# Kernel tuning notes

Measured on AMD Instinct MI355X. Metric: run time of the kernel, lower is better.

## Reference

```python
import jax, jax.numpy as jnp
import numpy as np
from jax import lax

DN = ('NCHW', 'OIHW', 'NCHW')

def _conv(x, w, b, stride, pad):
    y = lax.conv_general_dilated(x, w, (stride, stride), [(pad, pad), (pad, pad)], dimension_numbers=DN)
    return y + b[None, :, None, None]

def _resblock(x, w1, b1, w2, b2, wd, bd, stride):
    # standard pre-activation-free ResNet block: conv3x3(stride)-ReLU-conv3x3 + 1x1(stride) skip, final ReLU
    identity = _conv(x, wd, bd, stride, 0)
    h = jax.nn.relu(_conv(x, w1, b1, stride, 1))
    h = _conv(h, w2, b2, 1, 1)
    return jax.nn.relu(h + identity)

def _deconv(x, w, b, stride, out_pad):
    # PyTorch ConvTranspose2d(k=3, padding=1, output_padding=out_pad) as dilated conv
    # w has PyTorch layout (in_ch, out_ch, kH, kW) -> flip spatially, swap to OIHW
    wt = jnp.flip(w, (2, 3)).transpose(1, 0, 2, 3)
    y = lax.conv_general_dilated(x, wt, (1, 1), [(1, 1 + out_pad), (1, 1 + out_pad)], lhs_dilation=(stride, stride), dimension_numbers=DN)
    return y + b[None, :, None, None]

def _quantize(enc, codebook):
    # enc: (B, C, H, W); codebook: (N, C). Squared-Euclidean distances, argmin, lookup.
    e = enc.transpose(0, 2, 3, 1)  # (B, H, W, C)
    d = (jnp.sum(e * e, axis=-1, keepdims=True)
         - 2.0 * jnp.einsum('bhwc,nc->bhwn', e, codebook)
         + jnp.sum(codebook * codebook, axis=-1))  # (B, H, W, N)
    idx = jnp.argmin(d, axis=-1)
    q = codebook[idx]  # (B, H, W, C)
    return q.transpose(0, 3, 1, 2)

def setup_inputs() -> dict:
    key = jax.random.key(0)
    ks = jax.random.split(key, 28)
    def W(k, shape):
        return jax.random.normal(k, shape, jnp.float32) * 0.05
    inp = {"x": jax.random.normal(ks[0], (32, 3, 256, 256), jnp.float32)}
    enc_chans = [(3, 64), (64, 128), (128, 64)]
    i = 1
    for l, (cin, cout) in enumerate(enc_chans):
        inp[f"enc{l}_w1"] = W(ks[i], (cout, cin, 3, 3))
        inp[f"enc{l}_b1"] = W(ks[i + 1], (cout,))
        inp[f"enc{l}_w2"] = W(ks[i + 2], (cout, cout, 3, 3))
        inp[f"enc{l}_b2"] = W(ks[i + 3], (cout,))
        inp[f"enc{l}_wd"] = W(ks[i + 4], (cout, cin, 1, 1))
        inp[f"enc{l}_bd"] = W(ks[i + 5], (cout,))
        i += 6
    # decoder ConvTranspose2d weights in PyTorch layout (in_ch, out_ch, 3, 3)
    dec_chans = [(64, 128), (128, 64), (64, 3)]
    for l, (cin, cout) in enumerate(dec_chans):
        inp[f"dec{l}_w"] = W(ks[i], (cin, cout, 3, 3))
        inp[f"dec{l}_b"] = W(ks[i + 1], (cout,))
        i += 2
    inp["codebook"] = W(ks[i], (512, 64))
    return inp

def reference(x, enc0_w1, enc0_b1, enc0_w2, enc0_b2, enc0_wd, enc0_bd,
              enc1_w1, enc1_b1, enc1_w2, enc1_b2, enc1_wd, enc1_bd,
              enc2_w1, enc2_b1, enc2_w2, enc2_b2, enc2_wd, enc2_bd,
              dec0_w, dec0_b, dec1_w, dec1_b, dec2_w, dec2_b, codebook):
    # encode: 256 -> 128 -> 64 -> 64 spatially
    h = _resblock(x, enc0_w1, enc0_b1, enc0_w2, enc0_b2, enc0_wd, enc0_bd, 2)
    h = _resblock(h, enc1_w1, enc1_b1, enc1_w2, enc1_b2, enc1_wd, enc1_bd, 2)
    h = _resblock(h, enc2_w1, enc2_b1, enc2_w2, enc2_b2, enc2_wd, enc2_bd, 1)
    q = _quantize(h, codebook)
    # decode with output_size matching encoder input shapes (output_padding: 0, 1, 1)
    h = jax.nn.relu(_deconv(q, dec0_w, dec0_b, 1, 0))   # 64 -> 64
    h = jax.nn.relu(_deconv(h, dec1_w, dec1_b, 2, 1))   # 64 -> 128
    return _deconv(h, dec2_w, dec2_b, 2, 1)             # 128 -> 256
```

## Files before the change

kernel.cpp:

```cpp
#include <hip/hip_runtime.h>
#include <cstddef>


typedef float v4f __attribute__((ext_vector_type(4)));
typedef _Float16 f16x8 __attribute__((ext_vector_type(8)));
typedef _Float16 f16x4 __attribute__((ext_vector_type(4)));

__device__ __forceinline__ void fma4(v4f& a, float p, const v4f& w) {
    a.x = fmaf(p, w.x, a.x); a.y = fmaf(p, w.y, a.y);
    a.z = fmaf(p, w.z, a.z); a.w = fmaf(p, w.w, a.w);
}

__global__ void repack_k(const float* __restrict__ src, float* __restrict__ dst,
                         int cout, int coutR, int cin, int flip, int deconv)
{
    int t = blockIdx.x * 256 + threadIdx.x;
    int tot = cin * 9 * cout;
    if (t >= tot) return;
    int co = t % cout; int k = (t / cout) % 9; int ci = t / (9 * cout);
    float v = 0.f;
    if (co < coutR) {
        int ks = flip ? 8 - k : k;
        v = deconv ? src[((size_t)ci * coutR + co) * 9 + ks]
                   : src[((size_t)co * cin + ci) * 9 + ks];
    }
    dst[t] = v;
}

__global__ void repackB16_k(const float* __restrict__ src, _Float16* __restrict__ bh,
                            _Float16* __restrict__ bl, int COUT, int CIN, int deconv)
{
    int t = blockIdx.x * 256 + threadIdx.x;
    int tot = 9 * CIN * COUT;
    if (t >= tot) return;
    int NGtot = COUT >> 4, C32 = CIN >> 5;
    int j = t & 7;
    int lane = (t >> 3) & 63;
    int blk = t >> 9;
    int ng = blk % NGtot; blk /= NGtot;
    int c32 = blk % C32;
    int tap = blk / C32;
    int co = ng * 16 + (lane & 15);
    int ci = c32 * 32 + ((lane >> 4) & 3) * 8 + j;
    float v = deconv ? src[((size_t)ci * COUT + co) * 9 + (8 - tap)]
                     : src[((size_t)co * CIN + ci) * 9 + tap];
    _Float16 h = (_Float16)v;
    _Float16 l = (_Float16)(v - (float)h);
    bh[t] = h; bl[t] = l;
}

__global__ void repackQ_k(const float* __restrict__ cb, _Float16* __restrict__ qb)
{
    int t = blockIdx.x * 256 + threadIdx.x;
    if (t >= 65536) return;
    int j = t & 7;
    int lane = (t >> 3) & 63;
    int hl = (t >> 9) & 1;
    int s = (t >> 10) & 1;
    int nt = t >> 11;
    int code = nt * 16 + (lane & 15);
    int ci = s * 32 + ((lane >> 4) & 3) * 8 + j;
    float v = cb[(size_t)code * 64 + ci];
    _Float16 h = (_Float16)v;
    qb[t] = hl ? (_Float16)(v - (float)h) : h;
}

__global__ void cbnorm_k(const float* __restrict__ cb, float* __restrict__ cn)
{
    int i = blockIdx.x * 256 + threadIdx.x;
    if (i >= 512) return;
    float s = 0.f;
#pragma unroll
    for (int j = 0; j < 64; ++j) { float v = cb[i * 64 + j]; s = fmaf(v, v, s); }
    cn[i] = s;
}

template<int CIN, bool RELU, int ADDMODE, bool CLIN, bool CLOUT>
__launch_bounds__(256, 2)
__global__ void mconv3s1_k(const float* __restrict__ in,
                           const _Float16* __restrict__ Bh, const _Float16* __restrict__ Bl,
                           const float* __restrict__ bias, float* __restrict__ out,
                           const float* __restrict__ addend,
                           int COUT, int H, int W)
{
    constexpr int C32 = CIN / 32;
    __shared__ __align__(16) unsigned char smBuf[76416];
    _Float16* AH = (_Float16*)smBuf;
    _Float16* AL = AH + 12960;
    _Float16* BW = AL + 12960;
    float* smO = (float*)smBuf;

    const int tid = threadIdx.x;
    const int lane = tid & 63, yb = tid >> 6;
    const int n16 = lane & 15, q = lane >> 4;

    int b = blockIdx.x;
    const int chunks = COUT >> 6;
    const int coch = b % chunks; b /= chunks;
    const int tX = W >> 4; const int tx = b % tX; b /= tX;
    const int tY = H >> 4; const int ty = b % tY; const int n = b / tY;
    const int x0 = tx * 16, y0 = ty * 16;
    const int NGtot = COUT >> 4;
    const int ngbase = coch * 4, cobase = coch * 64;

    v4f acc[4][4];
#pragma unroll
    for (int ng = 0; ng < 4; ++ng) {
        float bb = bias[cobase + ng * 16 + n16];
        v4f bv = {bb, bb, bb, bb};
#pragma unroll
        for (int mg = 0; mg < 4; ++mg) acc[mg][ng] = bv;
    }

    for (int c32 = 0; c32 < C32; ++c32) {
        __syncthreads();
        if (CLIN) {
            for (int u = tid; u < 2592; u += 256) {
                int cell = u >> 3, f4 = u & 7;
                int yy = cell / 18, xx = cell - yy * 18;
                int gy = y0 - 1 + yy, gx = x0 - 1 + xx;
                float4 v = make_float4(0.f, 0.f, 0.f, 0.f);
                if (gy >= 0 && gy < H && gx >= 0 && gx < W)
                    v = *(const float4*)&in[(((size_t)n * H + gy) * W + gx) * CIN + c32 * 32 + f4 * 4];
                f16x4 h4, l4;
                h4[0] = (_Float16)v.x; l4[0] = (_Float16)(v.x - (float)h4[0]);
                h4[1] = (_Float16)v.y; l4[1] = (_Float16)(v.y - (float)h4[1]);
                h4[2] = (_Float16)v.z; l4[2] = (_Float16)(v.z - (float)h4[2]);
                h4[3] = (_Float16)v.w; l4[3] = (_Float16)(v.w - (float)h4[3]);
                int a = (yy * 18 + xx) * 40 + f4 * 4;
                *(f16x4*)&AH[a] = h4; *(f16x4*)&AL[a] = l4;
            }
        } else {
            for (int u = tid; u < 10368; u += 256) {
                int ci = u / 324, rem = u - ci * 324;
                int yy = rem / 18, xx = rem - yy * 18;
                int gy = y0 - 1 + yy, gx = x0 - 1 + xx;
                float v = 0.f;
                if (gy >= 0 && gy < H && gx >= 0 && gx < W)
                    v = in[(((size_t)n * CIN + c32 * 32 + ci) * H + gy) * W + gx];
                _Float16 h = (_Float16)v;
                _Float16 l = (_Float16)(v - (float)h);
                int a = (yy * 18 + xx) * 40 + ci;
                AH[a] = h; AL[a] = l;
            }
        }
        for (int ky = 0; ky < 3; ++ky) {
            __syncthreads();
            for (int u = tid; u < 1536; u += 256) {
                int lu = u & 63;
                int rest = u >> 6;
                int hl = rest & 1; rest >>= 1;
                int ng = rest & 3;
                int tapL = rest >> 2;
                const uint4* srcp = (const uint4*)(hl ? Bl : Bh);
                size_t sidx = (((size_t)(ky * 3 + tapL) * C32 + c32) * NGtot + ngbase + ng) * 64 + lu;
                ((uint4*)BW)[u] = srcp[sidx];
            }
            __syncthreads();
#pragma unroll
            for (int kx = 0; kx < 3; ++kx) {
                f16x8 aH[4], aL[4];
#pragma unroll
                for (int mg = 0; mg < 4; ++mg) {
                    int aoff = ((4 * yb + mg + ky) * 18 + n16 + kx) * 40 + q * 8;
                    aH[mg] = *(const f16x8*)&AH[aoff];
                    aL[mg] = *(const f16x8*)&AL[aoff];
                }
#pragma unroll
                for (int ng = 0; ng < 4; ++ng) {
                    int boff = ((kx * 4 + ng) * 2) * 512 + lane * 8;
                    f16x8 bH = *(const f16x8*)&BW[boff];
                    f16x8 bL = *(const f16x8*)&BW[boff + 512];
#pragma unroll
                    for (int mg = 0; mg < 4; ++mg) {
                        acc[mg][ng] = __builtin_amdgcn_mfma_f32_16x16x32_f16(aH[mg], bH, acc[mg][ng], 0, 0, 0);
                        acc[mg][ng] = __builtin_amdgcn_mfma_f32_16x16x32_f16(aL[mg], bH, acc[mg][ng], 0, 0, 0);
                        acc[mg][ng] = __builtin_amdgcn_mfma_f32_16x16x32_f16(aH[mg], bL, acc[mg][ng], 0, 0, 0);
                    }
                }
            }
        }
    }

    __syncthreads();
#pragma unroll
    for (int mg = 0; mg < 4; ++mg)
#pragma unroll
        for (int ng = 0; ng < 4; ++ng) {
            int p = (4 * yb + mg) * 16 + q * 4;
            int co = ng * 16 + n16;
#pragma unroll
            for (int r = 0; r < 4; ++r)
                smO[co * 257 + p + r] = acc[mg][ng][r];
        }
    __syncthreads();
    if (CLOUT) {
        const int p = tid;
        const int py = p >> 4, px = p & 15;
        size_t cellBase = (((size_t)n * H + (y0 + py)) * W + (x0 + px)) * COUT + cobase;
        float* cellp = out + cellBase;
        const float* acell = (ADDMODE == 2) ? addend + cellBase : nullptr;
#pragma unroll
        for (int g = 0; g < 16; ++g) {
            float4 v;
            v.x = smO[(4 * g + 0) * 257 + p];
            v.y = smO[(4 * g + 1) * 257 + p];
            v.z = smO[(4 * g + 2) * 257 + p];
            v.w = smO[(4 * g + 3) * 257 + p];
            if (ADDMODE == 2) {
                float4 a4 = *(const float4*)&acell[4 * g];
                v.x += a4.x; v.y += a4.y; v.z += a4.z; v.w += a4.w;
            }
            if (RELU) {
                v.x = fmaxf(v.x, 0.f); v.y = fmaxf(v.y, 0.f);
                v.z = fmaxf(v.z, 0.f); v.w = fmaxf(v.w, 0.f);
            }
            *(float4*)&cellp[4 * g] = v;
        }
    } else {
        const size_t plane = (size_t)H * W;
        float* ob = out + ((size_t)n * COUT + cobase) * plane;
        const float* ab = (ADDMODE == 1) ? addend + ((size_t)n * COUT + cobase) * plane : nullptr;
#pragma unroll
        for (int k = 0; k < 64; ++k) {
            int e = tid + 256 * k;
            int co = e >> 8, p = e & 255;
            int py = p >> 4, px = p & 15;
            size_t g = (size_t)co * plane + (size_t)(y0 + py) * W + x0 + px;
            float v = smO[co * 257 + p];
            if (ADDMODE == 1) v += ab[g];
            if (RELU) v = fmaxf(v, 0.f);
            ob[g] = v;
        }
    }
}

template<int CIN, int NG, bool RELU>
__launch_bounds__(256, 2)
__global__ void mconv3s2_k(const float* __restrict__ in,
                           const _Float16* __restrict__ Bh, const _Float16* __restrict__ Bl,
                           const float* __restrict__ bias, float* __restrict__ out,
                           int COUT, int Hin, int Win)
{
    constexpr int C32 = CIN / 32;
    constexpr int ASZ = 9 * 2 * 17 * 40;
    __shared__ __align__(16) unsigned char smBuf[(2 * ASZ + NG * 1024) * 2];
    _Float16* AH = (_Float16*)smBuf;
    _Float16* AL = AH + ASZ;
    _Float16* BW = AL + ASZ;
    float* smO = (float*)smBuf;

    const int tid = threadIdx.x;
    const int lane = tid & 63, yb = tid >> 6;
    const int n16 = lane & 15, q = lane >> 4;

    const int Hout = Hin >> 1, Wout = Win >> 1;
    int b = blockIdx.x;
    const int chunks = COUT / (NG * 16);
    const int coch = b % chunks; b /= chunks;
    const int tX = Wout >> 4; const int tx = b % tX; b /= tX;
    const int tY = Hout >> 2; const int ty = b % tY; const int n = b / tY;
    const int x0 = tx * 16, y0 = ty * 4;
    const int gx0 = 2 * x0 - 1, gy0 = 2 * y0 - 1;
    const int NGtot = COUT >> 4;
    const int ngbase = coch * NG, cobase = coch * NG * 16;

    v4f acc[NG];
#pragma unroll
    for (int ng = 0; ng < NG; ++ng) {
        float bb = bias[cobase + ng * 16 + n16];
        v4f bv = {bb, bb, bb, bb};
        acc[ng] = bv;
    }

    for (int c32 = 0; c32 < C32; ++c32) {
        __syncthreads();
        for (int u = tid; u < 9504; u += 256) {
            int ci = u / 297, rem = u - ci * 297;
            int yy = rem / 33, xx = rem - yy * 33;
            int gy = gy0 + yy, gx = gx0 + xx;
            float v = 0.f;
            if (gy >= 0 && gy < Hin && gx >= 0 && gx < Win)
                v = in[(((size_t)n * CIN + c32 * 32 + ci) * Hin + gy) * Win + gx];
            _Float16 h = (_Float16)v;
            _Float16 l = (_Float16)(v - (float)h);
            int a = ((yy * 2 + (xx & 1)) * 17 + (xx >> 1)) * 40 + ci;
            AH[a] = h; AL[a] = l;
        }
#pragma unroll
        for (int ky = 0; ky < 3; ++ky) {
#pragma unroll
            for (int kx = 0; kx < 3; ++kx) {
                __syncthreads();
                for (int u = tid; u < NG * 128; u += 256) {
                    int lu = u & 63;
                    int rest = u >> 6;
                    int hl = rest & 1;
                    int ng = rest >> 1;
                    const uint4* srcp = (const uint4*)(hl ? Bl : Bh);
                    size_t sidx = (((size_t)(ky * 3 + kx) * C32 + c32) * NGtot + ngbase + ng) * 64 + lu;
                    ((uint4*)BW)[u] = srcp[sidx];
                }
                __syncthreads();
                const int par = kx & 1, xs = kx >> 1;
                int aoff = (((2 * yb + ky) * 2 + par) * 17 + n16 + xs) * 40 + q * 8;
                f16x8 aH = *(const f16x8*)&AH[aoff];
                f16x8 aL = *(const f16x8*)&AL[aoff];
#pragma unroll
                for (int ng = 0; ng < NG; ++ng) {
                    int boff = ng * 1024 + lane * 8;
                    f16x8 bH = *(const f16x8*)&BW[boff];
                    f16x8 bL = *(const f16x8*)&BW[boff + 512];
                    acc[ng] = __builtin_amdgcn_mfma_f32_16x16x32_f16(aH, bH, acc[ng], 0, 0, 0);
                    acc[ng] = __builtin_amdgcn_mfma_f32_16x16x32_f16(aL, bH, acc[ng], 0, 0, 0);
                    acc[ng] = __builtin_amdgcn_mfma_f32_16x16x32_f16(aH, bL, acc[ng], 0, 0, 0);
                }
            }
        }
    }

    __syncthreads();
#pragma unroll
    for (int ng = 0; ng < NG; ++ng) {
        int co = ng * 16 + n16;
        int p = yb * 16 + q * 4;
#pragma unroll
        for (int r = 0; r < 4; ++r)
            smO[co * 65 + p + r] = acc[ng][r];
    }
    __syncthreads();
    const int p2 = tid >> 2, s2 = tid & 3;
    const int py = p2 >> 4, px = p2 & 15;
    float* cellp = out + ((((size_t)n * Hout + (y0 + py)) * Wout + (x0 + px)) * COUT + s2 * 32);
#pragma unroll
    for (int k = 0; k < 8; ++k) {
        float4 v;
        v.x = smO[(s2 * 32 + 4 * k + 0) * 65 + p2];
        v.y = smO[(s2 * 32 + 4 * k + 1) * 65 + p2];
        v.z = smO[(s2 * 32 + 4 * k + 2) * 65 + p2];
        v.w = smO[(s2 * 32 + 4 * k + 3) * 65 + p2];
        if (RELU) {
            v.x = fmaxf(v.x, 0.f); v.y = fmaxf(v.y, 0.f);
            v.z = fmaxf(v.z, 0.f); v.w = fmaxf(v.w, 0.f);
        }
        *(float4*)&cellp[4 * k] = v;
    }
}

template<int CIN, bool RELU>
__launch_bounds__(256, 3)
__global__ void mdeconv2_k(const float* __restrict__ in,
                           const _Float16* __restrict__ Bh, const _Float16* __restrict__ Bl,
                           const float* __restrict__ bias, float* __restrict__ out,
                           int COUT, int Hin, int Win)
{
    constexpr int C32 = CIN / 32;
    __shared__ __align__(16) unsigned char smBuf[38976];
    _Float16* AH = (_Float16*)smBuf;
    _Float16* AL = AH + 3600;
    _Float16* BW = AL + 3600;
    float* smO = (float*)smBuf;

    const int tid = threadIdx.x;
    const int lane = tid & 63, yb = tid >> 6;
    const int n16 = lane & 15, q = lane >> 4;

    int b = blockIdx.x;
    const int chunks = COUT >> 6;
    const int coch = b % chunks; b /= chunks;
    const int tX = Win >> 4; const int tx = b % tX; b /= tX;
    const int tY = Hin >> 2; const int ty = b % tY; const int n = b / tY;
    const int x0 = tx * 16, y0 = ty * 4;
    const int NGtot = COUT >> 4;
    const int ngbase = coch * 4, cobase = coch * 64;

    v4f acc[4][4];
#pragma unroll
    for (int ng = 0; ng < 4; ++ng) {
        float bb = bias[cobase + ng * 16 + n16];
        v4f bv = {bb, bb, bb, bb};
#pragma unroll
        for (int ph = 0; ph < 4; ++ph) acc[ph][ng] = bv;
    }

    for (int c32 = 0; c32 < C32; ++c32) {
        __syncthreads();
        for (int u = tid; u < 680; u += 256) {
            int cell = u >> 3, f4 = u & 7;
            int yy = cell / 17, xx = cell - yy * 17;
            int gy = y0 + yy, gx = x0 + xx;
            float4 v = make_float4(0.f, 0.f, 0.f, 0.f);
            if (gy < Hin && gx < Win)
                v = *(const float4*)&in[(((size_t)n * Hin + gy) * Win + gx) * CIN + c32 * 32 + f4 * 4];
            f16x4 h4, l4;
            h4[0] = (_Float16)v.x; l4[0] = (_Float16)(v.x - (float)h4[0]);
            h4[1] = (_Float16)v.y; l4[1] = (_Float16)(v.y - (float)h4[1]);
            h4[2] = (_Float16)v.z; l4[2] = (_Float16)(v.z - (float)h4[2]);
            h4[3] = (_Float16)v.w; l4[3] = (_Float16)(v.w - (float)h4[3]);
            int a = (yy * 18 + xx) * 40 + f4 * 4;
            *(f16x4*)&AH[a] = h4; *(f16x4*)&AL[a] = l4;
        }
        for (int ky = 0; ky < 3; ++ky) {
            __syncthreads();
            for (int u = tid; u < 1536; u += 256) {
                int lu = u & 63;
                int rest = u >> 6;
                int hl = rest & 1; rest >>= 1;
                int ng = rest & 3;
                int tapL = rest >> 2;
                const uint4* srcp = (const uint4*)(hl ? Bl : Bh);
                size_t sidx = (((size_t)(ky * 3 + tapL) * C32 + c32) * NGtot + ngbase + ng) * 64 + lu;
                ((uint4*)BW)[u] = srcp[sidx];
            }
            __syncthreads();
            const int iy = (ky == 2) ? 1 : 0;
            const int phy = (ky == 1) ? 0 : 2;
#pragma unroll
            for (int kx = 0; kx < 3; ++kx) {
                const int ix = (kx == 2) ? 1 : 0;
                const int ph = phy + ((kx == 1) ? 0 : 1);
                int aoff = ((yb + iy) * 18 + n16 + ix) * 40 + q * 8;
                f16x8 aH = *(const f16x8*)&AH[aoff];
                f16x8 aL = *(const f16x8*)&AL[aoff];
#pragma unroll
                for (int ng = 0; ng < 4; ++ng) {
                    int boff = ((kx * 4 + ng) * 2) * 512 + lane * 8;
                    f16x8 bH = *(const f16x8*)&BW[boff];
                    f16x8 bL = *(const f16x8*)&BW[boff + 512];
                    acc[ph][ng] = __builtin_amdgcn_mfma_f32_16x16x32_f16(aH, bH, acc[ph][ng], 0, 0, 0);
                    acc[ph][ng] = __builtin_amdgcn_mfma_f32_16x16x32_f16(aL, bH, acc[ph][ng], 0, 0, 0);
                    acc[ph][ng] = __builtin_amdgcn_mfma_f32_16x16x32_f16(aH, bL, acc[ph][ng], 0, 0, 0);
                }
            }
        }
    }

    const int Wout = Win * 2;
    const size_t plane = (size_t)(Hin * 2) * (size_t)Wout;
    float* ob = out + ((size_t)n * COUT + cobase) * plane;
    const int oy0 = 2 * y0, ox0 = 2 * x0;
#pragma unroll
    for (int half = 0; half < 2; ++half) {
        __syncthreads();
#pragma unroll
        for (int ph = 0; ph < 4; ++ph) {
            const int dy = ph >> 1, dx = ph & 1;
#pragma unroll
            for (int g = 0; g < 2; ++g) {
                int ng = half * 2 + g;
#pragma unroll
                for (int r = 0; r < 4; ++r)
                    smO[(g * 16 + n16) * 257 + (2 * yb + dy) * 32 + 2 * (q * 4 + r) + dx] = acc[ph][ng][r];
            }
        }
        __syncthreads();
#pragma unroll
        for (int k = 0; k < 32; ++k) {
            int pos = tid;
            int oyl = pos >> 5, oxl = pos & 31;
            float v = smO[k * 257 + pos];
            if (RELU) v = fmaxf(v, 0.f);
            ob[(size_t)(half * 32 + k) * plane + (size_t)(oy0 + oyl) * Wout + ox0 + oxl] = v;
        }
    }
}

template<int CIN, int CB, bool RELU>
__launch_bounds__(256, 4)
__global__ void conv3s2_k(const float* __restrict__ in, const float* __restrict__ wp,
                          const float* __restrict__ bias, float* __restrict__ out,
                          int COUT, int Hin, int Win)
{
    constexpr int COC = 32;
    __shared__ float smIn[CB * 2178];
    __shared__ float smW[CB * 9 * COC];
    const int Hout = Hin >> 1, Wout = Win >> 1;
    const int tid = threadIdx.x;
    int b = blockIdx.x;
    const int chunks = COUT / COC;
    const int tX = Wout / 32, tY = Hout / 16;
    const int ch = b % chunks; b /= chunks;
    const int tx = b % tX; b /= tX;
    const int ty = b % tY; const int n = b / tY;
    const int cobase = ch * COC;
    const int r = tid >> 4, c = tid & 15;
    const int gy0 = ty * 32 - 1, gx0 = tx * 64 - 1;

    v4f acc[16];
#pragma unroll
    for (int g = 0; g < 8; ++g) {
        v4f bv = *(const v4f*)&bias[cobase + 4 * g];
        acc[g] = bv; acc[8 + g] = bv;
    }

    const size_t plane = (size_t)Hin * Win;
    const float* ip0 = in + (size_t)n * CIN * plane;
    const float* wp0 = wp + cobase;

    for (int ci0 = 0; ci0 < CIN; ci0 += CB) {
        __syncthreads();
        for (int idx = tid; idx < CB * 2178; idx += 256) {
            int ci = idx / 2178, rem = idx - ci * 2178;
            int rr = rem / 66, cc = rem - rr * 66;
            int gy = gy0 + rr, gx = gx0 + cc;
            float v = 0.f;
            if (gy >= 0 && gy < Hin && gx >= 0 && gx < Win)
                v = ip0[(size_t)(ci0 + ci) * plane + (size_t)gy * Win + gx];
            smIn[idx] = v;
        }
        for (int idx = tid; idx < CB * 9 * COC; idx += 256) {
            int q2 = idx >> 5, co = idx & 31;
            smW[idx] = wp0[((size_t)ci0 * 9 + q2) * COUT + co];
        }
        __syncthreads();

#pragma unroll 1
        for (int ci = 0; ci < CB; ++ci) {
            float p[15];
            const float* sp = &smIn[ci * 2178 + 2 * r * 66 + 4 * c];
#pragma unroll
            for (int i = 0; i < 3; ++i)
#pragma unroll
                for (int j = 0; j < 5; ++j)
                    p[i * 5 + j] = sp[i * 66 + j];
            const float* wrow = &smW[ci * 288];
#pragma unroll
            for (int k = 0; k < 9; ++k) {
                const int ky = k / 3, kx = k % 3;
#pragma unroll
                for (int g = 0; g < 8; ++g) {
                    v4f wv = *(const v4f*)&wrow[k * 32 + 4 * g];
                    fma4(acc[g],     p[ky * 5 + kx],     wv);
                    fma4(acc[8 + g], p[ky * 5 + kx + 2], wv);
                }
            }
        }
    }

    const int oy = ty * 16 + r, ox = tx * 32 + 2 * c;
    size_t cellBase = (((size_t)n * Hout + oy) * Wout + ox) * COUT + cobase;
#pragma unroll
    for (int g = 0; g < 8; ++g) {
        v4f v0 = acc[g], v1 = acc[8 + g];
        if (RELU) {
#pragma unroll
            for (int e = 0; e < 4; ++e) { v0[e] = fmaxf(v0[e], 0.f); v1[e] = fmaxf(v1[e], 0.f); }
        }
        *(v4f*)&out[cellBase + 4 * g] = v0;
        *(v4f*)&out[cellBase + COUT + 4 * g] = v1;
    }
}

template<int CIN, int CB, int COC, bool RELU>
__launch_bounds__(256, 3)
__global__ void deconv2_k(const float* __restrict__ in, const float* __restrict__ wp,
                          const float* __restrict__ bias, float* __restrict__ out,
                          int COUTR, int COUTP, int Hin, int Win)
{
    constexpr int RW = 33, RH = 17;
    __shared__ float smIn[CB * RH * RW];
    __shared__ float smW[CB * 9 * COC];
    const int Wout = Win * 2;
    const int tid = threadIdx.x;
    int b = blockIdx.x;
    const int chunks = COUTP / COC;
    const int qTX = Win / 32, qTY = Hin / 16;
    const int ch = b % chunks; b /= chunks;
    const int qtx = b % qTX; b /= qTX;
    const int qty = b % qTY; const int n = b / qTY;
    const int cobase = ch * COC;
    const int tqy = tid >> 4, tqx = tid & 15;
    const int qby = qty * 16, qbx = qtx * 32;

    v4f acc[8 * COC / 4];
#pragma unroll
    for (int g = 0; g < COC / 4; ++g) {
        v4f bv;
#pragma unroll
        for (int e = 0; e < 4; ++e)
            bv[e] = (cobase + 4 * g + e < COUTR) ? bias[cobase + 4 * g + e] : 0.f;
#pragma unroll
        for (int pt = 0; pt < 8; ++pt) acc[pt * (COC / 4) + g] = bv;
    }

    const size_t plane = (size_t)Hin * Win;
    const float* ip0 = in + (size_t)n * CIN * plane;
    const float* wp0 = wp + cobase;

    for (int ci0 = 0; ci0 < CIN; ci0 += CB) {
        __syncthreads();
        for (int idx = tid; idx < CB * RH * RW; idx += 256) {
            int ci = idx / (RH * RW), rem = idx - ci * (RH * RW);
            int rr = rem / RW, cc = rem - rr * RW;
            int gy = qby + rr, gx = qbx + cc;
            float v = 0.f;
            if (gy < Hin && gx < Win)
                v = ip0[(size_t)(ci0 + ci) * plane + (size_t)gy * Win + gx];
            smIn[idx] = v;
        }
        for (int idx = tid; idx < CB * 9 * COC; idx += 256) {
            int q2 = idx / COC, co = idx % COC;
            smW[idx] = wp0[((size_t)ci0 * 9 + q2) * COUTP + co];
        }
        __syncthreads();

#pragma unroll 1
        for (int ci = 0; ci < CB; ++ci) {
            float p[6];
            const float* sp = &smIn[ci * RH * RW + tqy * RW + 2 * tqx];
#pragma unroll
            for (int i = 0; i < 2; ++i)
#pragma unroll
                for (int j = 0; j < 3; ++j)
                    p[i * 3 + j] = sp[i * RW + j];
            const float* wrow = &smW[ci * 9 * COC];
#pragma unroll
            for (int k = 0; k < 9; ++k) {
                const int ky = k / 3, kx = k % 3;
                const int dy = (ky == 1) ? 0 : 1, iy = (ky == 0) ? 1 : 0;
                const int dx = (kx == 1) ? 0 : 1, ix = (kx == 0) ? 1 : 0;
#pragma unroll
                for (int g = 0; g < COC / 4; ++g) {
                    v4f wv = *(const v4f*)&wrow[k * COC + 4 * g];
                    fma4(acc[(0 + dy * 2 + dx) * (COC / 4) + g], p[iy * 3 + ix],     wv);
                    fma4(acc[(4 + dy * 2 + dx) * (COC / 4) + g], p[iy * 3 + ix + 1], wv);
                }
            }
        }
    }

    const size_t oPlane = (size_t)(Hin * 2) * Wout;
    const int oy = 2 * (qby + tqy), ox = 2 * (qbx + 2 * tqx);
#pragma unroll
    for (int g = 0; g < COC / 4; ++g)
#pragma unroll
        for (int e = 0; e < 4; ++e) {
            int cch = cobase + 4 * g + e;
            if (cch >= COUTR) break;
            float* op = out + ((size_t)n * COUTR + cch) * oPlane + (size_t)oy * Wout + ox;
#pragma unroll
            for (int a2 = 0; a2 < 2; ++a2) {
                float u0 = acc[(0 + a2 * 2 + 0) * (COC / 4) + g][e];
                float u1 = acc[(0 + a2 * 2 + 1) * (COC / 4) + g][e];
                float u2 = acc[(4 + a2 * 2 + 0) * (COC / 4) + g][e];
                float u3 = acc[(4 + a2 * 2 + 1) * (COC / 4) + g][e];
                if (RELU) { u0 = fmaxf(u0, 0.f); u1 = fmaxf(u1, 0.f);
                            u2 = fmaxf(u2, 0.f); u3 = fmaxf(u3, 0.f); }
                *(float4*)&op[(size_t)a2 * Wout] = make_float4(u0, u1, u2, u3);
            }
        }
}

template<int CIN, int S, bool RELU, bool CLOUT>
__launch_bounds__(256, 4)
__global__ void conv1x1_k(const float* __restrict__ in, const float* __restrict__ w,
                          const float* __restrict__ bias, float* __restrict__ out,
                          int COUT, int Hin, int Win, int Hout, int Wout)
{
    constexpr int COC = 32;
    __shared__ float smW[CIN * COC];
    const int tid = threadIdx.x;
    int b = blockIdx.x;
    const int chunks = COUT / COC;
    const int spB = (Hout * Wout) / 256;
    const int ch = b % chunks; b /= chunks;
    const int sb = b % spB; const int n = b / spB;
    const int cobase = ch * COC;

    for (int idx = tid; idx < CIN * COC; idx += 256) {
        int ci = idx / COC, co = idx - ci * COC;
        smW[idx] = w[(size_t)(cobase + co) * CIN + ci];
    }
    __syncthreads();

    const int pos = sb * 256 + tid;
    const int oy = pos / Wout, ox = pos - oy * Wout;

    v4f acc[8];
#pragma unroll
    for (int g = 0; g < 8; ++g) acc[g] = *(const v4f*)&bias[cobase + 4 * g];

    const size_t inPlane = (size_t)Hin * Win;
    const float* ip = in + (size_t)n * CIN * inPlane + (size_t)(oy * S) * Win + (size_t)(ox * S);
#pragma unroll 1
    for (int ci = 0; ci < CIN; ++ci) {
        float v = ip[(size_t)ci * inPlane];
#pragma unroll
        for (int g = 0; g < 8; ++g)
            fma4(acc[g], v, *(const v4f*)&smW[ci * COC + 4 * g]);
    }
    const size_t outPlane = (size_t)Hout * Wout;
    if (CLOUT) {
        size_t cb2 = ((size_t)n * outPlane + pos) * COUT + cobase;
#pragma unroll
        for (int g = 0; g < 8; ++g) {
            v4f v = acc[g];
            if (RELU) {
#pragma unroll
                for (int e = 0; e < 4; ++e) v[e] = fmaxf(v[e], 0.f);
            }
            *(v4f*)&out[cb2 + 4 * g] = v;
        }
    } else {
        float* op = out + ((size_t)n * COUT + cobase) * outPlane + pos;
#pragma unroll
        for (int g = 0; g < 8; ++g)
#pragma unroll
            for (int e = 0; e < 4; ++e) {
                float v = acc[g][e];
                if (RELU) v = fmaxf(v, 0.f);
                op[(size_t)(4 * g + e) * outPlane] = v;
            }
    }
}

__launch_bounds__(256, 4)
__global__ void mquant_k(const float* __restrict__ h, const _Float16* __restrict__ QB,
                         const float* __restrict__ cn, const float* __restrict__ cb,
                         float* __restrict__ q)
{
    __shared__ __align__(16) _Float16 AF[2][8192];
    __shared__ float cns[512];
    __shared__ int bidxs[128];

    const int tid = threadIdx.x;
    const int lane = tid & 63;
    const int wv = tid >> 6;
    const int n16 = lane & 15, qq = lane >> 4;

    const int n = blockIdx.x >> 5;
    const int rem0 = (blockIdx.x & 31) << 7;

    for (int u = tid; u < 1024; u += 256) {
        int posL = u >> 3, grp = u & 7;
        const float* gp = h + ((size_t)n * 4096 + rem0 + posL) * 64 + grp * 8;
        float4 v0 = *(const float4*)gp;
        float4 v1 = *(const float4*)(gp + 4);
        f16x8 hh, ll;
        hh[0] = (_Float16)v0.x; ll[0] = (_Float16)(v0.x - (float)hh[0]);
        hh[1] = (_Float16)v0.y; ll[1] = (_Float16)(v0.y - (float)hh[1]);
        hh[2] = (_Float16)v0.z; ll[2] = (_Float16)(v0.z - (float)hh[2]);
        hh[3] = (_Float16)v0.w; ll[3] = (_Float16)(v0.w - (float)hh[3]);
        hh[4] = (_Float16)v1.x; ll[4] = (_Float16)(v1.x - (float)hh[4]);
        hh[5] = (_Float16)v1.y; ll[5] = (_Float16)(v1.y - (float)hh[5]);
        hh[6] = (_Float16)v1.z; ll[6] = (_Float16)(v1.z - (float)hh[6]);
        hh[7] = (_Float16)v1.w; ll[7] = (_Float16)(v1.w - (float)hh[7]);
        int mt = posL >> 4, s = grp >> 2, qv = grp & 3;
        int a = ((mt * 2 + s) * 64 + (posL & 15) + qv * 16) * 8;
        *(f16x8*)&AF[0][a] = hh;
        *(f16x8*)&AF[1][a] = ll;
    }
    for (int u = tid; u < 512; u += 256) cns[u] = cn[u];
    __syncthreads();

    f16x8 aH[2][2], aL[2][2];
#pragma unroll
    for (int m = 0; m < 2; ++m)
#pragma unroll
        for (int s = 0; s < 2; ++s) {
            int a = (((wv * 2 + m) * 2 + s) * 64 + lane) * 8;
            aH[m][s] = *(const f16x8*)&AF[0][a];
            aL[m][s] = *(const f16x8*)&AF[1][a];
        }

    float best[2][4]; int bi[2][4];
#pragma unroll
    for (int m = 0; m < 2; ++m)
#pragma unroll
        for (int r = 0; r < 4; ++r) { best[m][r] = 3.4e38f; bi[m][r] = 0; }

    const uint4* qbp = (const uint4*)QB;
#pragma unroll 1
    for (int nt = 0; nt < 32; ++nt) {
        uint4 rH0 = qbp[((nt * 2 + 0) * 2 + 0) * 64 + lane];
        uint4 rL0 = qbp[((nt * 2 + 0) * 2 + 1) * 64 + lane];
        uint4 rH1 = qbp[((nt * 2 + 1) * 2 + 0) * 64 + lane];
        uint4 rL1 = qbp[((nt * 2 + 1) * 2 + 1) * 64 + lane];
        f16x8 bH0 = *(const f16x8*)&rH0;
        f16x8 bL0 = *(const f16x8*)&rL0;
        f16x8 bH1 = *(const f16x8*)&rH1;
        f16x8 bL1 = *(const f16x8*)&rL1;
        float cnv = cns[nt * 16 + n16];
        const int code = nt * 16 + n16;
#pragma unroll
        for (int m = 0; m < 2; ++m) {
            v4f acc = {0.f, 0.f, 0.f, 0.f};
            acc = __builtin_amdgcn_mfma_f32_16x16x32_f16(aH[m][0], bH0, acc, 0, 0, 0);
            acc = __builtin_amdgcn_mfma_f32_16x16x32_f16(aL[m][0], bH0, acc, 0, 0, 0);
            acc = __builtin_amdgcn_mfma_f32_16x16x32_f16(aH[m][0], bL0, acc, 0, 0, 0);
            acc = __builtin_amdgcn_mfma_f32_16x16x32_f16(aH[m][1], bH1, acc, 0, 0, 0);
            acc = __builtin_amdgcn_mfma_f32_16x16x32_f16(aL[m][1], bH1, acc, 0, 0, 0);
            acc = __builtin_amdgcn_mfma_f32_16x16x32_f16(aH[m][1], bL1, acc, 0, 0, 0);
#pragma unroll
            for (int r = 0; r < 4; ++r) {
                float d = fmaf(-2.f, acc[r], cnv);
                if (d < best[m][r]) { best[m][r] = d; bi[m][r] = code; }
            }
        }
    }

#pragma unroll
    for (int m = 0; m < 2; ++m)
#pragma unroll
        for (int r = 0; r < 4; ++r) {
#pragma unroll
            for (int msk = 1; msk < 16; msk <<= 1) {
                float ob = __shfl_xor(best[m][r], msk);
                int oi = __shfl_xor(bi[m][r], msk);
                if (ob < best[m][r] || (ob == best[m][r] && oi < bi[m][r])) {
                    best[m][r] = ob; bi[m][r] = oi;
                }
            }
            if (n16 == 0) bidxs[wv * 32 + m * 16 + qq * 4 + r] = bi[m][r];
        }
    __syncthreads();

    const int p = tid & 127, jh = tid >> 7;
    const int code = bidxs[p];
    const float4* crow4 = (const float4*)(cb + (size_t)code * 64);
    float4* qp4 = (float4*)(q + ((size_t)n * 4096 + rem0 + p) * 64);
#pragma unroll
    for (int k = 0; k < 8; ++k)
        qp4[jh * 8 + k] = crow4[jh * 8 + k];
}

extern "C" void kernel_launch(void* const* d_in, const int* in_sizes, int n_in,
                              void* d_out, int out_size, void* d_ws, size_t ws_size,
                              hipStream_t stream)
{
    const float* x    = (const float*)d_in[0];
    const float* e0w1 = (const float*)d_in[1];  const float* e0b1 = (const float*)d_in[2];
    const float* e0w2 = (const float*)d_in[3];  const float* e0b2 = (const float*)d_in[4];
    const float* e0wd = (const float*)d_in[5];  const float* e0bd = (const float*)d_in[6];
    const float* e1w1 = (const float*)d_in[7];  const float* e1b1 = (const float*)d_in[8];
    const float* e1w2 = (const float*)d_in[9];  const float* e1b2 = (const float*)d_in[10];
    const float* e1wd = (const float*)d_in[11]; const float* e1bd = (const float*)d_in[12];
    const float* e2w1 = (const float*)d_in[13]; const float* e2b1 = (const float*)d_in[14];
    const float* e2w2 = (const float*)d_in[15]; const float* e2b2 = (const float*)d_in[16];
    const float* e2wd = (const float*)d_in[17]; const float* e2bd = (const float*)d_in[18];
    const float* d0w  = (const float*)d_in[19]; const float* d0b  = (const float*)d_in[20];
    const float* d1w  = (const float*)d_in[21]; const float* d1b  = (const float*)d_in[22];
    const float* d2w  = (const float*)d_in[23]; const float* d2b  = (const float*)d_in[24];
    const float* cb   = (const float*)d_in[25];
    float* out = (float*)d_out;
    float* ws  = (float*)d_ws;

    float* P_e0w1 = out + 0;
    _Float16* Bh_d1   = (_Float16*)(out + 1728);
    _Float16* Bl_d1   = (_Float16*)(out + 38592);
    _Float16* Bh_e0c2 = (_Float16*)(out + 77760);
    _Float16* Bl_e0c2 = (_Float16*)(out + 96192);
    _Float16* Bh_e1c2 = (_Float16*)(out + 114624);
    _Float16* Bl_e1c2 = (_Float16*)(out + 188352);
    _Float16* Bh_e2c1 = (_Float16*)(out + 262080);
    _Float16* Bl_e2c1 = (_Float16*)(out + 298944);
    _Float16* Bh_e2c2 = (_Float16*)(out + 335808);
    _Float16* Bl_e2c2 = (_Float16*)(out + 354240);
    _Float16* Bh_d0   = (_Float16*)(out + 372672);
    _Float16* Bl_d0   = (_Float16*)(out + 409536);
    _Float16* Bh_e1c1 = (_Float16*)(out + 446400);
    _Float16* Bl_e1c1 = (_Float16*)(out + 483264);
    _Float16* QB = (_Float16*)(out + 520128);
    float* CN = out + 552896;
    float* P_d2w  = ws + 50405376;

    float* S0 = ws;
    float* T1 = ws + 33554432;
    float* T3 = ws + 33554432;
    float* S1 = ws + 50331648;
    float* S2 = ws;
    float* T5 = ws + 8388608;
    float* Q  = ws + 16777216;
    float* D0 = ws + 33554432;
    float* D1 = ws;

    dim3 blk(256);
    auto rp = [&](const float* src, float* dst, int cout, int coutR, int cin, int flip, int dec) {
        int tot = cin * 9 * cout;
        repack_k<<<dim3((tot + 255) / 256), blk, 0, stream>>>(src, dst, cout, coutR, cin, flip, dec);
    };
    auto rpB = [&](const float* src, _Float16* bh, _Float16* bl, int cout, int cin, int dec) {
        int tot = 9 * cin * cout;
        repackB16_k<<<dim3((tot + 255) / 256), blk, 0, stream>>>(src, bh, bl, cout, cin, dec);
    };

    rp(e0w1, P_e0w1, 64, 64, 3, 0, 0);
    rpB(e0w2, Bh_e0c2, Bl_e0c2, 64, 64, 0);
    rpB(e1w1, Bh_e1c1, Bl_e1c1, 128, 64, 0);
    rpB(e1w2, Bh_e1c2, Bl_e1c2, 128, 128, 0);
    rpB(e2w1, Bh_e2c1, Bl_e2c1, 64, 128, 0);
    rpB(e2w2, Bh_e2c2, Bl_e2c2, 64, 64, 0);
    rpB(d0w,  Bh_d0,   Bl_d0,   128, 64, 1);
    rpB(d1w,  Bh_d1,   Bl_d1,   64, 128, 1);
    repackQ_k<<<dim3(256), blk, 0, stream>>>(cb, QB);
    cbnorm_k<<<dim3(2), blk, 0, stream>>>(cb, CN);

    conv1x1_k<3, 2, false, false><<<dim3(32 * 64 * 2), blk, 0, stream>>>(
        x, e0wd, e0bd, S0, 64, 256, 256, 128, 128);
    conv3s2_k<3, 3, true><<<dim3(32 * 8 * 4 * 2), blk, 0, stream>>>(
        x, P_e0w1, e0b1, T1, 64, 256, 256);
    mconv3s1_k<64, true, 1, true, false><<<dim3(32 * 8 * 8 * 1), blk, 0, stream>>>(
        T1, Bh_e0c2, Bl_e0c2, e0b2, S0, S0, 64, 128, 128);

    conv1x1_k<64, 2, false, false><<<dim3(32 * 16 * 4), blk, 0, stream>>>(
        S0, e1wd, e1bd, S1, 128, 128, 128, 64, 64);
    mconv3s2_k<64, 8, true><<<dim3(32 * 16 * 4), blk, 0, stream>>>(
        S0, Bh_e1c1, Bl_e1c1, e1b1, T3, 128, 128, 128);
    mconv3s1_k<128, true, 1, true, false><<<dim3(32 * 4 * 4 * 2), blk, 0, stream>>>(
        T3, Bh_e1c2, Bl_e1c2, e1b2, S1, S1, 128, 64, 64);

    conv1x1_k<128, 1, false, true><<<dim3(32 * 16 * 2), blk, 0, stream>>>(
        S1, e2wd, e2bd, S2, 64, 64, 64, 64, 64);
    mconv3s1_k<128, true, 0, false, true><<<dim3(32 * 4 * 4 * 1), blk, 0, stream>>>(
        S1, Bh_e2c1, Bl_e2c1, e2b1, T5, nullptr, 64, 64, 64);
    rp(d2w, P_d2w, 4, 3, 64, 0, 1);
    mconv3s1_k<64, true, 2, true, true><<<dim3(32 * 4 * 4 * 1), blk, 0, stream>>>(
        T5, Bh_e2c2, Bl_e2c2, e2b2, S2, S2, 64, 64, 64);

    mquant_k<<<dim3(1024), blk, 0, stream>>>(S2, QB, CN, cb, Q);

    mconv3s1_k<64, true, 0, true, true><<<dim3(32 * 4 * 4 * 2), blk, 0, stream>>>(
        Q, Bh_d0, Bl_d0, d0b, D0, nullptr, 128, 64, 64);

    mdeconv2_k<128, true><<<dim3(32 * 16 * 4), blk, 0, stream>>>(
        D0, Bh_d1, Bl_d1, d1b, D1, 64, 64, 64);

    deconv2_k<64, 8, 4, false><<<dim3(32 * 4 * 8), blk, 0, stream>>>(
        D1, P_d2w, d2b, out, 3, 4, 128, 128);
}
```

Measured before the change: 1.518 ms.

## Switch encoder intermediates to channels-last and stream conv weights from global

Encoder residual outputs S0 and S1 are now written channels-last, so the strided 3x3 MFMA conv and the 1x1 skip convs read them with float4 loads along channels instead of scalar strided loads. The strided conv also stops staging weight tiles in shared memory every tap, which drops two barriers per tap, and reads the fp16 hi/lo weights straight from global. It raises the occupancy hint to 3 blocks. The cost is more global/L2 weight traffic per wave and a layout change that ties several kernels' template flags together.

```diff
diff --git a/kernel.cpp b/kernel.cpp
--- a/kernel.cpp
+++ b/kernel.cpp
@@ -236,7 +236,7 @@
 }
 
 template<int CIN, int NG, bool RELU>
-__launch_bounds__(256, 2)
+__launch_bounds__(256, 3)
 __global__ void mconv3s2_k(const float* __restrict__ in,
                            const _Float16* __restrict__ Bh, const _Float16* __restrict__ Bl,
                            const float* __restrict__ bias, float* __restrict__ out,
@@ -244,10 +244,9 @@
 {
     constexpr int C32 = CIN / 32;
     constexpr int ASZ = 9 * 2 * 17 * 40;
-    __shared__ __align__(16) unsigned char smBuf[(2 * ASZ + NG * 1024) * 2];
+    __shared__ __align__(16) unsigned char smBuf[2 * ASZ * 2];
     _Float16* AH = (_Float16*)smBuf;
     _Float16* AL = AH + ASZ;
-    _Float16* BW = AL + ASZ;
     float* smO = (float*)smBuf;
 
     const int tid = threadIdx.x;
@@ -273,44 +272,42 @@
         acc[ng] = bv;
     }
 
+    const uint4* bhp = (const uint4*)Bh;
+    const uint4* blp = (const uint4*)Bl;
+
     for (int c32 = 0; c32 < C32; ++c32) {
         __syncthreads();
-        for (int u = tid; u < 9504; u += 256) {
-            int ci = u / 297, rem = u - ci * 297;
-            int yy = rem / 33, xx = rem - yy * 33;
+        for (int u = tid; u < 2376; u += 256) {
+            int cell = u >> 3, f4 = u & 7;
+            int yy = cell / 33, xx = cell - yy * 33;
             int gy = gy0 + yy, gx = gx0 + xx;
-            float v = 0.f;
+            float4 v = make_float4(0.f, 0.f, 0.f, 0.f);
             if (gy >= 0 && gy < Hin && gx >= 0 && gx < Win)
-                v = in[(((size_t)n * CIN + c32 * 32 + ci) * Hin + gy) * Win + gx];
-            _Float16 h = (_Float16)v;
-            _Float16 l = (_Float16)(v - (float)h);
-            int a = ((yy * 2 + (xx & 1)) * 17 + (xx >> 1)) * 40 + ci;
-            AH[a] = h; AL[a] = l;
-        }
+                v = *(const float4*)&in[(((size_t)n * Hin + gy) * Win + gx) * CIN + c32 * 32 + f4 * 4];
+            f16x4 h4, l4;
+            h4[0] = (_Float16)v.x; l4[0] = (_Float16)(v.x - (float)h4[0]);
+            h4[1] = (_Float16)v.y; l4[1] = (_Float16)(v.y - (float)h4[1]);
+            h4[2] = (_Float16)v.z; l4[2] = (_Float16)(v.z - (float)h4[2]);
+            h4[3] = (_Float16)v.w; l4[3] = (_Float16)(v.w - (float)h4[3]);
+            int a = ((yy * 2 + (xx & 1)) * 17 + (xx >> 1)) * 40 + f4 * 4;
+            *(f16x4*)&AH[a] = h4; *(f16x4*)&AL[a] = l4;
+        }
+        __syncthreads();
 #pragma unroll
         for (int ky = 0; ky < 3; ++ky) {
 #pragma unroll
             for (int kx = 0; kx < 3; ++kx) {
-                __syncthreads();
-                for (int u = tid; u < NG * 128; u += 256) {
-                    int lu = u & 63;
-                    int rest = u >> 6;
-                    int hl = rest & 1;
-                    int ng = rest >> 1;
-                    const uint4* srcp = (const uint4*)(hl ? Bl : Bh);
-                    size_t sidx = (((size_t)(ky * 3 + kx) * C32 + c32) * NGtot + ngbase + ng) * 64 + lu;
-                    ((uint4*)BW)[u] = srcp[sidx];
-                }
-                __syncthreads();
                 const int par = kx & 1, xs = kx >> 1;
                 int aoff = (((2 * yb + ky) * 2 + par) * 17 + n16 + xs) * 40 + q * 8;
                 f16x8 aH = *(const f16x8*)&AH[aoff];
                 f16x8 aL = *(const f16x8*)&AL[aoff];
+                size_t sb0 = (((size_t)(ky * 3 + kx) * C32 + c32) * NGtot + ngbase) * 64 + lane;
 #pragma unroll
                 for (int ng = 0; ng < NG; ++ng) {
-                    int boff = ng * 1024 + lane * 8;
-                    f16x8 bH = *(const f16x8*)&BW[boff];
-                    f16x8 bL = *(const f16x8*)&BW[boff + 512];
+                    uint4 rH = bhp[sb0 + (size_t)ng * 64];
+                    uint4 rL = blp[sb0 + (size_t)ng * 64];
+                    f16x8 bH = *(const f16x8*)&rH;
+                    f16x8 bL = *(const f16x8*)&rL;
                     acc[ng] = __builtin_amdgcn_mfma_f32_16x16x32_f16(aH, bH, acc[ng], 0, 0, 0);
                     acc[ng] = __builtin_amdgcn_mfma_f32_16x16x32_f16(aL, bH, acc[ng], 0, 0, 0);
                     acc[ng] = __builtin_amdgcn_mfma_f32_16x16x32_f16(aH, bL, acc[ng], 0, 0, 0);
@@ -651,7 +648,7 @@
         }
 }
 
-template<int CIN, int S, bool RELU, bool CLOUT>
+template<int CIN, int S, bool RELU, bool CLIN, bool CLOUT>
 __launch_bounds__(256, 4)
 __global__ void conv1x1_k(const float* __restrict__ in, const float* __restrict__ w,
                           const float* __restrict__ bias, float* __restrict__ out,
@@ -680,14 +677,27 @@
 #pragma unroll
     for (int g = 0; g < 8; ++g) acc[g] = *(const v4f*)&bias[cobase + 4 * g];
 
-    const size_t inPlane = (size_t)Hin * Win;
-    const float* ip = in + (size_t)n * CIN * inPlane + (size_t)(oy * S) * Win + (size_t)(ox * S);
+    if (CLIN) {
+        const float* ip = in + (((size_t)n * Hin + oy * S) * Win + ox * S) * CIN;
 #pragma unroll 1
-    for (int ci = 0; ci < CIN; ++ci) {
-        float v = ip[(size_t)ci * inPlane];
-#pragma unroll
-        for (int g = 0; g < 8; ++g)
-            fma4(acc[g], v, *(const v4f*)&smW[ci * COC + 4 * g]);
+        for (int c4 = 0; c4 < CIN / 4; ++c4) {
+            v4f v = *(const v4f*)&ip[c4 * 4];
+#pragma unroll
+            for (int e = 0; e < 4; ++e)
+#pragma unroll
+                for (int g = 0; g < 8; ++g)
+                    fma4(acc[g], v[e], *(const v4f*)&smW[(c4 * 4 + e) * COC + 4 * g]);
+        }
+    } else {
+        const size_t inPlane = (size_t)Hin * Win;
+        const float* ip = in + (size_t)n * CIN * inPlane + (size_t)(oy * S) * Win + (size_t)(ox * S);
+#pragma unroll 1
+        for (int ci = 0; ci < CIN; ++ci) {
+            float v = ip[(size_t)ci * inPlane];
+#pragma unroll
+            for (int g = 0; g < 8; ++g)
+                fma4(acc[g], v, *(const v4f*)&smW[ci * COC + 4 * g]);
+        }
     }
     const size_t outPlane = (size_t)Hout * Wout;
     if (CLOUT) {
@@ -895,23 +905,23 @@
     repackQ_k<<<dim3(256), blk, 0, stream>>>(cb, QB);
     cbnorm_k<<<dim3(2), blk, 0, stream>>>(cb, CN);
 
-    conv1x1_k<3, 2, false, false><<<dim3(32 * 64 * 2), blk, 0, stream>>>(
+    conv1x1_k<3, 2, false, false, true><<<dim3(32 * 64 * 2), blk, 0, stream>>>(
         x, e0wd, e0bd, S0, 64, 256, 256, 128, 128);
     conv3s2_k<3, 3, true><<<dim3(32 * 8 * 4 * 2), blk, 0, stream>>>(
         x, P_e0w1, e0b1, T1, 64, 256, 256);
-    mconv3s1_k<64, true, 1, true, false><<<dim3(32 * 8 * 8 * 1), blk, 0, stream>>>(
+    mconv3s1_k<64, true, 2, true, true><<<dim3(32 * 8 * 8 * 1), blk, 0, stream>>>(
         T1, Bh_e0c2, Bl_e0c2, e0b2, S0, S0, 64, 128, 128);
 
-    conv1x1_k<64, 2, false, false><<<dim3(32 * 16 * 4), blk, 0, stream>>>(
+    conv1x1_k<64, 2, false, true, true><<<dim3(32 * 16 * 4), blk, 0, stream>>>(
         S0, e1wd, e1bd, S1, 128, 128, 128, 64, 64);
     mconv3s2_k<64, 8, true><<<dim3(32 * 16 * 4), blk, 0, stream>>>(
         S0, Bh_e1c1, Bl_e1c1, e1b1, T3, 128, 128, 128);
-    mconv3s1_k<128, true, 1, true, false><<<dim3(32 * 4 * 4 * 2), blk, 0, stream>>>(
+    mconv3s1_k<128, true, 2, true, true><<<dim3(32 * 4 * 4 * 2), blk, 0, stream>>>(
         T3, Bh_e1c2, Bl_e1c2, e1b2, S1, S1, 128, 64, 64);
 
-    conv1x1_k<128, 1, false, true><<<dim3(32 * 16 * 2), blk, 0, stream>>>(
+    conv1x1_k<128, 1, false, true, true><<<dim3(32 * 16 * 2), blk, 0, stream>>>(
         S1, e2wd, e2bd, S2, 64, 64, 64, 64, 64);
-    mconv3s1_k<128, true, 0, false, true><<<dim3(32 * 4 * 4 * 1), blk, 0, stream>>>(
+    mconv3s1_k<128, true, 0, true, true><<<dim3(32 * 4 * 4 * 1), blk, 0, stream>>>(
         S1, Bh_e2c1, Bl_e2c1, e2b1, T5, nullptr, 64, 64, 64);
     rp(d2w, P_d2w, 4, 3, 64, 0, 1);
     mconv3s1_k<64, true, 2, true, true><<<dim3(32 * 4 * 4 * 1), blk, 0, stream>>>(
```

Result: no change. 1.510 ms (-0.5%).
